# Performance work log

Hardware: AMD Instinct MI355X
Metric: run time of the kernel (lower is better)

The kernel has to match this reference:

```python
import jax, jax.numpy as jnp
import numpy as np

B, N, C = 4, 4096, 128  # batch, tokens (flattened 3D volume), channels
F = 128  # filters


def setup_inputs() -> dict:
    key = jax.random.key(0)
    ks = jax.random.split(key, 7)
    s = 1.0 / np.sqrt(C)
    return {
        "inputs": jax.random.normal(ks[0], (B, N, C), dtype=jnp.float32),
        "Wq": jax.random.normal(ks[1], (C, F), dtype=jnp.float32) * s,
        "bq": jnp.zeros((F,), dtype=jnp.float32),
        "Wk": jax.random.normal(ks[2], (C, F), dtype=jnp.float32) * s,
        "bk": jnp.zeros((F,), dtype=jnp.float32),
        "Wv": jax.random.normal(ks[3], (C, F), dtype=jnp.float32) * s,
        "bv": jnp.zeros((F,), dtype=jnp.float32),
    }


def reference(inputs, Wq, bq, Wk, bk, Wv, bv):
    # Dense projections
    q = inputs @ Wq + bq  # [B, N, F]
    k = inputs @ Wk + bk
    v = inputs @ Wv + bv
    scale = jnp.sqrt(jnp.asarray(F, dtype=q.dtype))
    scores = jnp.einsum("bnf,bmf->bnm", q, k) / scale  # [B, N, N]
    weights = jax.nn.softmax(scores, axis=-1)
    return jnp.einsum("bnm,bmf->bnf", weights, v)
```

## Files before the change

### kernel.cpp

```cpp
#include <hip/hip_runtime.h>

typedef unsigned short u16;
typedef unsigned int u32;
typedef float f32x4 __attribute__((ext_vector_type(4)));
typedef short s16x8 __attribute__((ext_vector_type(8)));
typedef unsigned int u32x2 __attribute__((ext_vector_type(2)));
typedef unsigned int u32x4 __attribute__((ext_vector_type(4)));

#define NB 4
#define NT 4096
#define ND 128
#define NQ (NB * NT)

#define QK_SCALE 0.12751879523138906f

using as3_void = __attribute__((address_space(3))) void;
using as1_void = __attribute__((address_space(1))) void;

__device__ __forceinline__ u16 f2bf(float x){
  unsigned u = __float_as_uint(x);
  return (u16)((u + 0x7FFFu + ((u >> 16) & 1u)) >> 16);
}
__device__ __forceinline__ u32 cvtpk(float lo, float hi){
  u32 r; asm("v_cvt_pk_bf16_f32 %0, %1, %2" : "=v"(r) : "v"(lo), "v"(hi)); return r;
}
__device__ __forceinline__ f32x4 mfma16(s16x8 a, s16x8 b, f32x4 c){
  return __builtin_amdgcn_mfma_f32_16x16x32_bf16(a, b, c, 0, 0, 0);
}

__global__ void k_wprep(const float* __restrict__ Wq, const float* __restrict__ Wk,
                        const float* __restrict__ Wv, u16* __restrict__ WT){
  int mat = blockIdx.x >> 7;
  int f   = blockIdx.x & 127;
  const float* W = (mat == 0) ? Wq : (mat == 1) ? Wk : Wv;
  int c = threadIdx.x;
  WT[mat * 16384 + f * 128 + c] = f2bf(W[c * 128 + f]);
}

__global__ __launch_bounds__(256) void k_proj(
    const float* __restrict__ X, const u16* __restrict__ WT,
    const float* __restrict__ bq, const float* __restrict__ bk, const float* __restrict__ bv,
    u16* __restrict__ Qs, u16* __restrict__ Ks, u16* __restrict__ VTs)
{
  const int lane = threadIdx.x & 63;
  const int w    = threadIdx.x >> 6;
  const int lm = lane & 15, lg = lane >> 4;
  const int rowbase = blockIdx.x * 64 + w * 16;

  s16x8 a[4];
  const float* xr = X + (rowbase + lm) * ND;
  #pragma unroll
  for (int kc = 0; kc < 4; ++kc){
    f32x4 x0 = *(const f32x4*)(xr + kc * 32 + lg * 8);
    f32x4 x1 = *(const f32x4*)(xr + kc * 32 + lg * 8 + 4);
    s16x8 t;
    t[0]=(short)f2bf(x0[0]); t[1]=(short)f2bf(x0[1]); t[2]=(short)f2bf(x0[2]); t[3]=(short)f2bf(x0[3]);
    t[4]=(short)f2bf(x1[0]); t[5]=(short)f2bf(x1[1]); t[6]=(short)f2bf(x1[2]); t[7]=(short)f2bf(x1[3]);
    a[kc] = t;
  }

  #pragma unroll
  for (int mat = 0; mat < 3; ++mat){
    const float* bias = (mat==0) ? bq : (mat==1) ? bk : bv;
    float bl[8];
    #pragma unroll
    for (int n = 0; n < 8; ++n) bl[n] = bias[n * 16 + lm];
    f32x4 acc[8];
    #pragma unroll
    for (int n = 0; n < 8; ++n) acc[n] = f32x4{0.f,0.f,0.f,0.f};
    #pragma unroll
    for (int kc = 0; kc < 4; ++kc){
      #pragma unroll
      for (int n = 0; n < 8; ++n){
        s16x8 bf = *(const s16x8*)&WT[mat*16384 + (n*16 + lm)*128 + kc*32 + lg*8];
        acc[n] = mfma16(a[kc], bf, acc[n]);
      }
    }
    #pragma unroll
    for (int n = 0; n < 8; ++n){
      int f = n * 16 + lm;
      #pragma unroll
      for (int i = 0; i < 4; ++i){
        int r = rowbase + lg * 4 + i;
        float val = acc[n][i] + bl[n];
        if (mat == 0){
          Qs[r * ND + f] = f2bf(val * QK_SCALE);
        } else if (mat == 1){
          Ks[r * ND + (f ^ ((r & 7) << 3))] = f2bf(val);
        } else {
          int bb = r >> 12, nt = r & (NT - 1);
          VTs[(bb * ND + f) * NT + (nt ^ ((f & 3) << 3) ^ (((f >> 2) & 1) << 2))] = f2bf(val);
        }
      }
    }
  }
}

__global__ __launch_bounds__(512, 2) void k_attn(
    const u16* __restrict__ Qs, const u16* __restrict__ Ks,
    const u16* __restrict__ VTs, float* __restrict__ Op, float* __restrict__ lp)
{
  __shared__ __align__(16) u16 lds[49152];
  __shared__ float lbuf[4][32];
  u16* kbuf = lds;
  u16* vbuf = lds + 24576;

  const int lin = blockIdx.x;
  const int logical = (lin & 7) * 32 + (lin >> 3);
  const int qblk = logical & 127;
  const int half = logical >> 7;

  const int lane = threadIdx.x & 63;
  const int w  = threadIdx.x >> 6;
  const int g  = w & 1, qw = w >> 1;
  const int lm = lane & 15, lg = lane >> 4;
  const int q0 = qblk * 128 + qw * 32;
  const int b  = q0 >> 12;
  const int kv0 = half * 2048 + g * 1024;

  s16x8 aq[2][4];
  #pragma unroll
  for (int sq = 0; sq < 2; ++sq){
    const u16* qr = Qs + (size_t)(q0 + sq * 16 + lm) * ND;
    #pragma unroll
    for (int kc = 0; kc < 4; ++kc) aq[sq][kc] = *(const s16x8*)(qr + kc * 32 + lg * 8);
  }

  f32x4 o[2][8];
  #pragma unroll
  for (int sq = 0; sq < 2; ++sq)
    #pragma unroll
    for (int n = 0; n < 8; ++n) o[sq][n] = f32x4{0.f,0.f,0.f,0.f};
  float l_[2] = {0.f, 0.f};

  const u16* gk = Ks  + ((size_t)b * NT + kv0 + qw * 8 + (lane >> 4)) * ND + (lane & 15) * 8;
  const u16* gv = VTs + ((size_t)b * ND + qw * 32 + (lane >> 2)) * NT + kv0 + (lane & 3) * 8;

  auto stage = [&](int buf){
    u16* kd = kbuf + (buf * 2 + g) * 4096 + qw * 1024;
    u16* vd = vbuf + (buf * 2 + g) * 4096 + qw * 1024;
    __builtin_amdgcn_global_load_lds((const as1_void*)gk,
                                     (as3_void*)kd, 16, 0, 0);
    __builtin_amdgcn_global_load_lds((const as1_void*)(gk + (size_t)4 * ND),
                                     (as3_void*)(kd + 512), 16, 0, 0);
    __builtin_amdgcn_global_load_lds((const as1_void*)gv,
                                     (as3_void*)vd, 16, 0, 0);
    __builtin_amdgcn_global_load_lds((const as1_void*)(gv + (size_t)16 * NT),
                                     (as3_void*)(vd + 512), 16, 0, 0);
    gk += (size_t)32 * ND;
    gv += 32;
  };

  const int kswz = (lm & 7) << 3;
  const int vswz = ((lm & 3) << 3) ^ (((lm >> 2) & 1) << 2);
  const int vcol0 = (lg * 4) ^ vswz;
  const int vcol1 = (16 + lg * 4) ^ vswz;

  stage(0);
  stage(1);
  int bufr = 0, bufs = 2;

  for (int t = 0; t < 32; ++t){
    if (t < 31) asm volatile("s_waitcnt vmcnt(4)" ::: "memory");
    else        asm volatile("s_waitcnt vmcnt(0)" ::: "memory");
    __builtin_amdgcn_sched_barrier(0);
    __builtin_amdgcn_s_barrier();
    __builtin_amdgcn_sched_barrier(0);

    if (t < 30){
      stage(bufs);
      bufs = (bufs == 2) ? 0 : bufs + 1;
    }

    const u16* kb = kbuf + (bufr * 2 + g) * 4096;
    const u16* vb = vbuf + (bufr * 2 + g) * 4096;

    f32x4 st[2][2];
    #pragma unroll
    for (int sq = 0; sq < 2; ++sq)
      #pragma unroll
      for (int n = 0; n < 2; ++n) st[sq][n] = f32x4{0.f,0.f,0.f,0.f};
    __builtin_amdgcn_s_setprio(1);
    #pragma unroll
    for (int kc = 0; kc < 4; ++kc){
      #pragma unroll
      for (int n = 0; n < 2; ++n){
        s16x8 kf = *(const s16x8*)&kb[(n * 16 + lm) * 128 + ((kc * 32 + lg * 8) ^ kswz)];
        st[0][n] = mfma16(kf, aq[0][kc], st[0][n]);
        st[1][n] = mfma16(kf, aq[1][kc], st[1][n]);
      }
    }
    __builtin_amdgcn_s_setprio(0);

    s16x8 pa[2];
    #pragma unroll
    for (int sq = 0; sq < 2; ++sq){
      float p[8];
      #pragma unroll
      for (int n = 0; n < 2; ++n)
        #pragma unroll
        for (int i = 0; i < 4; ++i){
          p[n * 4 + i] = __builtin_amdgcn_exp2f(st[sq][n][i]);
          l_[sq] += p[n * 4 + i];
        }
      pa[sq] = __builtin_bit_cast(s16x8, u32x4{
          cvtpk(p[0], p[1]), cvtpk(p[2], p[3]),
          cvtpk(p[4], p[5]), cvtpk(p[6], p[7])});
    }

    __builtin_amdgcn_s_setprio(1);
    #pragma unroll
    for (int nf = 0; nf < 8; ++nf){
      const int vr = (nf * 16 + lm) * 32;
      u32x2 v0 = *(const u32x2*)&vb[vr + vcol0];
      u32x2 v1 = *(const u32x2*)&vb[vr + vcol1];
      s16x8 vf = __builtin_bit_cast(s16x8, u32x4{v0[0], v0[1], v1[0], v1[1]});
      o[0][nf] = mfma16(pa[0], vf, o[0][nf]);
      o[1][nf] = mfma16(pa[1], vf, o[1][nf]);
    }
    __builtin_amdgcn_s_setprio(0);

    bufr = (bufr == 2) ? 0 : bufr + 1;
  }

  #pragma unroll
  for (int sq = 0; sq < 2; ++sq){
    float v = l_[sq];
    v += __shfl_xor(v, 16);
    v += __shfl_xor(v, 32);
    l_[sq] = v;
  }

  float* mbF = (float*)lds;
  __syncthreads();
  if (g == 1){
    #pragma unroll
    for (int sq = 0; sq < 2; ++sq){
      #pragma unroll
      for (int i = 0; i < 4; ++i)
        #pragma unroll
        for (int nf = 0; nf < 8; ++nf)
          mbF[qw * 4096 + (sq * 16 + lg * 4 + i) * 128 + nf * 16 + lm] = o[sq][nf][i];
      if (lg == 0) lbuf[qw][sq * 16 + lm] = l_[sq];
    }
  }
  __syncthreads();
  if (g == 0){
    #pragma unroll
    for (int sq = 0; sq < 2; ++sq){
      l_[sq] += lbuf[qw][sq * 16 + lm];
      #pragma unroll
      for (int i = 0; i < 4; ++i){
        const size_t r = (size_t)half * NQ + q0 + sq * 16 + lg * 4 + i;
        #pragma unroll
        for (int nf = 0; nf < 8; ++nf)
          Op[r * ND + nf * 16 + lm] =
              o[sq][nf][i] + mbF[qw * 4096 + (sq * 16 + lg * 4 + i) * 128 + nf * 16 + lm];
      }
      if (lg == 0) lp[(size_t)half * NQ + q0 + sq * 16 + lm] = l_[sq];
    }
  }
}

__global__ __launch_bounds__(256) void k_merge(const float* __restrict__ Op,
                                               const float* __restrict__ lp,
                                               float* __restrict__ Out){
  const int gid = blockIdx.x * 256 + threadIdx.x;
  const int q = gid >> 5, c = gid & 31;
  f32x4 a = *(const f32x4*)(Op + (size_t)q * ND + c * 4);
  f32x4 d = *(const f32x4*)(Op + ((size_t)NQ + q) * ND + c * 4);
  const float inv = 1.f / (lp[q] + lp[NQ + q]);
  f32x4 r;
  r[0] = (a[0] + d[0]) * inv; r[1] = (a[1] + d[1]) * inv;
  r[2] = (a[2] + d[2]) * inv; r[3] = (a[3] + d[3]) * inv;
  *(f32x4*)(Out + (size_t)q * ND + c * 4) = r;
}

extern "C" void kernel_launch(void* const* d_in, const int* in_sizes, int n_in,
                              void* d_out, int out_size, void* d_ws, size_t ws_size,
                              hipStream_t stream) {
  const float* X  = (const float*)d_in[0];
  const float* Wq = (const float*)d_in[1];
  const float* bq = (const float*)d_in[2];
  const float* Wk = (const float*)d_in[3];
  const float* bk = (const float*)d_in[4];
  const float* Wv = (const float*)d_in[5];
  const float* bv = (const float*)d_in[6];
  float* Out = (float*)d_out;

  u16* Qs  = (u16*)d_ws;
  u16* Ks  = Qs  + (size_t)NQ * ND;
  u16* VTs = Ks  + (size_t)NQ * ND;
  u16* WT  = VTs + (size_t)NQ * ND;
  float* Op = (float*)(WT + 3 * 128 * 128);
  float* lp = Op + (size_t)2 * NQ * ND;

  hipLaunchKernelGGL(k_wprep, dim3(3 * 128), dim3(128), 0, stream, Wq, Wk, Wv, WT);
  hipLaunchKernelGGL(k_proj,  dim3(NQ / 64), dim3(256), 0, stream,
                     X, WT, bq, bk, bv, Qs, Ks, VTs);
  hipLaunchKernelGGL(k_attn,  dim3(256), dim3(512), 0, stream, Qs, Ks, VTs, Op, lp);
  hipLaunchKernelGGL(k_merge, dim3(NQ * 32 / 256), dim3(256), 0, stream, Op, lp, Out);
}
```

Before: 85.69 us.

## Split attention KV range four ways with bf16 partials and double buffering

After: 80.93 us. -5.6%, faster.

```diff
diff --git a/kernel.cpp b/kernel.cpp
--- a/kernel.cpp
+++ b/kernel.cpp
@@ -96,27 +96,27 @@
   }
 }
 
-__global__ __launch_bounds__(512, 2) void k_attn(
+__global__ __launch_bounds__(512, 4) void k_attn(
     const u16* __restrict__ Qs, const u16* __restrict__ Ks,
-    const u16* __restrict__ VTs, float* __restrict__ Op, float* __restrict__ lp)
+    const u16* __restrict__ VTs, u16* __restrict__ Op, float* __restrict__ lp)
 {
-  __shared__ __align__(16) u16 lds[49152];
+  __shared__ __align__(16) u16 lds[32768];
   __shared__ float lbuf[4][32];
   u16* kbuf = lds;
-  u16* vbuf = lds + 24576;
+  u16* vbuf = lds + 16384;
 
   const int lin = blockIdx.x;
-  const int logical = (lin & 7) * 32 + (lin >> 3);
+  const int logical = (lin & 7) * 64 + (lin >> 3);
   const int qblk = logical & 127;
-  const int half = logical >> 7;
+  const int quarter = logical >> 7;
 
   const int lane = threadIdx.x & 63;
   const int w  = threadIdx.x >> 6;
-  const int g  = w & 1, qw = w >> 1;
+  const int qw = w >> 1, g = w & 1;
   const int lm = lane & 15, lg = lane >> 4;
   const int q0 = qblk * 128 + qw * 32;
   const int b  = q0 >> 12;
-  const int kv0 = half * 2048 + g * 1024;
+  const int kv0 = quarter * 1024 + g * 512;
 
   s16x8 aq[2][4];
   #pragma unroll
@@ -157,23 +157,13 @@
   const int vcol1 = (16 + lg * 4) ^ vswz;
 
   stage(0);
-  stage(1);
-  int bufr = 0, bufs = 2;
-
-  for (int t = 0; t < 32; ++t){
-    if (t < 31) asm volatile("s_waitcnt vmcnt(4)" ::: "memory");
-    else        asm volatile("s_waitcnt vmcnt(0)" ::: "memory");
-    __builtin_amdgcn_sched_barrier(0);
-    __builtin_amdgcn_s_barrier();
-    __builtin_amdgcn_sched_barrier(0);
-
-    if (t < 30){
-      stage(bufs);
-      bufs = (bufs == 2) ? 0 : bufs + 1;
-    }
-
-    const u16* kb = kbuf + (bufr * 2 + g) * 4096;
-    const u16* vb = vbuf + (bufr * 2 + g) * 4096;
+  __syncthreads();
+  int par = 0;
+
+  for (int t = 0; t < 16; ++t){
+    if (t < 15) stage(par ^ 1);
+    const u16* kb = kbuf + (par * 2 + g) * 4096;
+    const u16* vb = vbuf + (par * 2 + g) * 4096;
 
     f32x4 st[2][2];
     #pragma unroll
@@ -220,7 +210,8 @@
     }
     __builtin_amdgcn_s_setprio(0);
 
-    bufr = (bufr == 2) ? 0 : bufr + 1;
+    __syncthreads();
+    par ^= 1;
   }
 
   #pragma unroll
@@ -251,29 +242,35 @@
       l_[sq] += lbuf[qw][sq * 16 + lm];
       #pragma unroll
       for (int i = 0; i < 4; ++i){
-        const size_t r = (size_t)half * NQ + q0 + sq * 16 + lg * 4 + i;
+        const size_t r = (size_t)quarter * NQ + q0 + sq * 16 + lg * 4 + i;
         #pragma unroll
         for (int nf = 0; nf < 8; ++nf)
-          Op[r * ND + nf * 16 + lm] =
-              o[sq][nf][i] + mbF[qw * 4096 + (sq * 16 + lg * 4 + i) * 128 + nf * 16 + lm];
+          Op[r * ND + nf * 16 + lm] = f2bf(
+              o[sq][nf][i] + mbF[qw * 4096 + (sq * 16 + lg * 4 + i) * 128 + nf * 16 + lm]);
       }
-      if (lg == 0) lp[(size_t)half * NQ + q0 + sq * 16 + lm] = l_[sq];
-    }
-  }
-}
-
-__global__ __launch_bounds__(256) void k_merge(const float* __restrict__ Op,
+      if (lg == 0) lp[(size_t)quarter * NQ + q0 + sq * 16 + lm] = l_[sq];
+    }
+  }
+}
+
+__global__ __launch_bounds__(256) void k_merge(const u16* __restrict__ Op,
                                                const float* __restrict__ lp,
                                                float* __restrict__ Out){
   const int gid = blockIdx.x * 256 + threadIdx.x;
-  const int q = gid >> 5, c = gid & 31;
-  f32x4 a = *(const f32x4*)(Op + (size_t)q * ND + c * 4);
-  f32x4 d = *(const f32x4*)(Op + ((size_t)NQ + q) * ND + c * 4);
-  const float inv = 1.f / (lp[q] + lp[NQ + q]);
-  f32x4 r;
-  r[0] = (a[0] + d[0]) * inv; r[1] = (a[1] + d[1]) * inv;
-  r[2] = (a[2] + d[2]) * inv; r[3] = (a[3] + d[3]) * inv;
-  *(f32x4*)(Out + (size_t)q * ND + c * 4) = r;
+  const int q = gid >> 4, c = gid & 15;
+  const float inv = 1.f / (lp[q] + lp[NQ + q] + lp[2 * NQ + q] + lp[3 * NQ + q]);
+  float acc[8] = {0,0,0,0,0,0,0,0};
+  #pragma unroll
+  for (int qt = 0; qt < 4; ++qt){
+    s16x8 v = *(const s16x8*)(Op + ((size_t)qt * NQ + q) * ND + c * 8);
+    #pragma unroll
+    for (int j = 0; j < 8; ++j)
+      acc[j] += __uint_as_float(((u32)(u16)v[j]) << 16);
+  }
+  f32x4 r0{acc[0]*inv, acc[1]*inv, acc[2]*inv, acc[3]*inv};
+  f32x4 r1{acc[4]*inv, acc[5]*inv, acc[6]*inv, acc[7]*inv};
+  *(f32x4*)(Out + (size_t)q * ND + c * 8)     = r0;
+  *(f32x4*)(Out + (size_t)q * ND + c * 8 + 4) = r1;
 }
 
 extern "C" void kernel_launch(void* const* d_in, const int* in_sizes, int n_in,
@@ -292,12 +289,12 @@
   u16* Ks  = Qs  + (size_t)NQ * ND;
   u16* VTs = Ks  + (size_t)NQ * ND;
   u16* WT  = VTs + (size_t)NQ * ND;
-  float* Op = (float*)(WT + 3 * 128 * 128);
-  float* lp = Op + (size_t)2 * NQ * ND;
+  u16* Op  = WT + 3 * 128 * 128;
+  float* lp = (float*)(Op + (size_t)4 * NQ * ND);
 
   hipLaunchKernelGGL(k_wprep, dim3(3 * 128), dim3(128), 0, stream, Wq, Wk, Wv, WT);
   hipLaunchKernelGGL(k_proj,  dim3(NQ / 64), dim3(256), 0, stream,
                      X, WT, bq, bk, bv, Qs, Ks, VTs);
-  hipLaunchKernelGGL(k_attn,  dim3(256), dim3(512), 0, stream, Qs, Ks, VTs, Op, lp);
-  hipLaunchKernelGGL(k_merge, dim3(NQ * 32 / 256), dim3(256), 0, stream, Op, lp, Out);
-}
+  hipLaunchKernelGGL(k_attn,  dim3(512), dim3(512), 0, stream, Qs, Ks, VTs, Op, lp);
+  hipLaunchKernelGGL(k_merge, dim3(NQ * 16 / 256), dim3(256), 0, stream, Op, lp, Out);
+}
```
